# Optimization experiments

Measured on AMD Instinct MI355X. Metric: run time of the kernel, lower is better.

Reference implementation:

```python
import jax, jax.numpy as jnp
import numpy as np

QUANT_MIN = -128.0
QUANT_MAX = 127.0
EPS = 1.1920928955078125e-07  # torch.finfo(float32).eps, torchao default
STEPS = 100


def setup_inputs() -> dict:
    key = jax.random.key(0)
    x = jax.random.normal(key, (8192, 8192), dtype=jnp.float32)
    return {"x": x}


def _fake_quant_rows(x, thres):
    """Symmetric int8 fake-quant with per-row threshold.

    scale = thres / ((qmax - qmin)/2) clamped at eps, zero_point = 0.
    x: [N, K], thres: [N].
    """
    scale = jnp.maximum(thres / ((QUANT_MAX - QUANT_MIN) / 2.0), EPS)  # [N]
    s = scale[:, None]
    q = jnp.clip(jnp.round(x / s), QUANT_MIN, QUANT_MAX)
    return q * s  # dequant (zero_point == 0)


def reference(x):
    # PerAxis(axis=0): block (1, K) -> per-row stats, reduce over axis 1
    min_val = jnp.min(x, axis=1)                       # [N]
    max_val = jnp.max(x, axis=1)                       # [N]
    range_val = jnp.maximum(jnp.abs(min_val), max_val)  # [N]
    opt_loss = jnp.full_like(min_val, 1e9)

    def step(carry, i):
        min_v, max_v, opt = carry
        thres = range_val / STEPS * i                  # [N]
        xq = _fake_quant_rows(x, thres)                # [N, K]
        loss = jnp.mean(jnp.square(xq - x), axis=1)    # [N]
        better = loss < opt
        min_v = jnp.where(better, -thres, min_v)
        max_v = jnp.where(better, thres, max_v)
        opt = jnp.minimum(loss, opt)
        return (min_v, max_v, opt), None

    steps = jnp.arange(1, STEPS + 1, dtype=x.dtype)
    (min_val, max_val, _), _ = jax.lax.scan(step, (min_val, max_val, opt_loss), steps)
    return jnp.stack([min_val, max_val])  # [2, N]
```

## Files before the change

kernel.cpp:

```cpp
#include <hip/hip_runtime.h>

#define K 8192
#define NROWS 8192
#define NSTEPS 100
#define QEPS 1.1920928955078125e-07f

__global__ __launch_bounds__(256) void mse_observer_kernel(
    const float* __restrict__ x, float* __restrict__ out)
{
    const int row  = blockIdx.x;
    const int tid  = threadIdx.x;
    const int lane = tid & 63;
    const int wave = tid >> 6;

    const float4* xr = reinterpret_cast<const float4*>(x + (size_t)row * K);

    float xv[32];
    #pragma unroll
    for (int j = 0; j < 8; ++j) {
        float4 v = xr[tid + j * 256];
        xv[j * 4 + 0] = v.x;
        xv[j * 4 + 1] = v.y;
        xv[j * 4 + 2] = v.z;
        xv[j * 4 + 3] = v.w;
    }

    float vmin = xv[0], vmax = xv[0];
    #pragma unroll
    for (int e = 1; e < 32; ++e) {
        vmin = fminf(vmin, xv[e]);
        vmax = fmaxf(vmax, xv[e]);
    }
    #pragma unroll
    for (int off = 32; off >= 1; off >>= 1) {
        vmin = fminf(vmin, __shfl_xor(vmin, off));
        vmax = fmaxf(vmax, __shfl_xor(vmax, off));
    }

    __shared__ float smin[4], smax[4];
    __shared__ float partial[NSTEPS * 4];
    __shared__ float sloss[NSTEPS];

    if (lane == 0) { smin[wave] = vmin; smax[wave] = vmax; }
    __syncthreads();

    const float rmin  = fminf(fminf(smin[0], smin[1]), fminf(smin[2], smin[3]));
    const float rmax  = fmaxf(fmaxf(smax[0], smax[1]), fmaxf(smax[2], smax[3]));
    const float range = fmaxf(fabsf(rmin), rmax);
    const float rstep = range / (float)NSTEPS;

    for (int i = 1; i <= NSTEPS; ++i) {
        const float thres = rstep * (float)i;
        const float s     = fmaxf(thres / 127.5f, QEPS);
        const float inv_s = 1.0f / s;
        float acc = 0.0f;
        #pragma unroll
        for (int e = 0; e < 32; ++e) {
            float q = __builtin_amdgcn_fmed3f(
                __builtin_rintf(xv[e] * inv_s), -128.0f, 127.0f);
            float d = __builtin_fmaf(q, s, -xv[e]);
            acc = __builtin_fmaf(d, d, acc);
        }
        #pragma unroll
        for (int off = 32; off >= 1; off >>= 1) acc += __shfl_xor(acc, off);
        if (lane == 0) partial[(i - 1) * 4 + wave] = acc;
    }
    __syncthreads();

    if (tid < NSTEPS) {
        sloss[tid] = (partial[tid * 4 + 0] + partial[tid * 4 + 1]) +
                     (partial[tid * 4 + 2] + partial[tid * 4 + 3]);
    }
    __syncthreads();

    if (tid == 0) {
        float opt = 3.4e38f;
        int best = 0;
        #pragma unroll 1
        for (int i = 0; i < NSTEPS; ++i) {
            float l = sloss[i];
            if (l < opt) { opt = l; best = i; }
        }
        const float tbest = rstep * (float)(best + 1);
        out[row]         = -tbest;
        out[NROWS + row] =  tbest;
    }
}

extern "C" void kernel_launch(void* const* d_in, const int* in_sizes, int n_in,
                              void* d_out, int out_size, void* d_ws, size_t ws_size,
                              hipStream_t stream) {
    const float* x = (const float*)d_in[0];
    float* out = (float*)d_out;
    mse_observer_kernel<<<NROWS, 256, 0, stream>>>(x, out);
}
```

Baseline: 979.5 us.

## Stream row data from memory per pass over threshold chunks instead of holding it in registers

The row is no longer held in 32 registers. The 100 thresholds are split into 5 passes of 20, and each pass re-reads the row's float4 values from global memory (likely from cache) with a one-ahead prefetch. Each loaded element is reused across 20 accumulators, and the per-step scale and inverse are precomputed once into shared memory and broadcast with readfirstlane. The aim is to cut register pressure and the serialized per-step shuffle reductions, and to batch reductions so more independent work is in flight. The cost is five reloads of each row, which may add memory traffic if the cache does not hold the row.

```diff
diff --git a/kernel.cpp b/kernel.cpp
--- a/kernel.cpp
+++ b/kernel.cpp
@@ -3,7 +3,13 @@
 #define K 8192
 #define NROWS 8192
 #define NSTEPS 100
+#define CHUNK 20
+#define NPASS 5
 #define QEPS 1.1920928955078125e-07f
+
+__device__ __forceinline__ float rdfirst(float v) {
+    return __int_as_float(__builtin_amdgcn_readfirstlane(__float_as_int(v)));
+}
 
 __global__ __launch_bounds__(256) void mse_observer_kernel(
     const float* __restrict__ x, float* __restrict__ out)
@@ -13,23 +19,15 @@
     const int lane = tid & 63;
     const int wave = tid >> 6;
 
-    const float4* xr = reinterpret_cast<const float4*>(x + (size_t)row * K);
+    const float4* __restrict__ xr =
+        reinterpret_cast<const float4*>(x + (size_t)row * K);
 
-    float xv[32];
+    float vmin =  3.4e38f, vmax = -3.4e38f;
     #pragma unroll
     for (int j = 0; j < 8; ++j) {
         float4 v = xr[tid + j * 256];
-        xv[j * 4 + 0] = v.x;
-        xv[j * 4 + 1] = v.y;
-        xv[j * 4 + 2] = v.z;
-        xv[j * 4 + 3] = v.w;
-    }
-
-    float vmin = xv[0], vmax = xv[0];
-    #pragma unroll
-    for (int e = 1; e < 32; ++e) {
-        vmin = fminf(vmin, xv[e]);
-        vmax = fmaxf(vmax, xv[e]);
+        vmin = fminf(vmin, fminf(fminf(v.x, v.y), fminf(v.z, v.w)));
+        vmax = fmaxf(vmax, fmaxf(fmaxf(v.x, v.y), fmaxf(v.z, v.w)));
     }
     #pragma unroll
     for (int off = 32; off >= 1; off >>= 1) {
@@ -37,9 +35,10 @@
         vmax = fmaxf(vmax, __shfl_xor(vmax, off));
     }
 
-    __shared__ float smin[4], smax[4];
-    __shared__ float partial[NSTEPS * 4];
-    __shared__ float sloss[NSTEPS];
+    __shared__ float  smin[4], smax[4];
+    __shared__ float2 sitab[NSTEPS];
+    __shared__ float  partial[NSTEPS * 4];
+    __shared__ float  sloss[NSTEPS];
 
     if (lane == 0) { smin[wave] = vmin; smax[wave] = vmax; }
     __syncthreads();
@@ -49,21 +48,54 @@
     const float range = fmaxf(fabsf(rmin), rmax);
     const float rstep = range / (float)NSTEPS;
 
-    for (int i = 1; i <= NSTEPS; ++i) {
-        const float thres = rstep * (float)i;
+    if (tid < NSTEPS) {
+        const float thres = rstep * (float)(tid + 1);
         const float s     = fmaxf(thres / 127.5f, QEPS);
-        const float inv_s = 1.0f / s;
-        float acc = 0.0f;
+        sitab[tid] = make_float2(s, 1.0f / s);
+    }
+    __syncthreads();
+
+    #pragma unroll 1
+    for (int p = 0; p < NPASS; ++p) {
+        float ss[CHUNK], si[CHUNK];
         #pragma unroll
-        for (int e = 0; e < 32; ++e) {
-            float q = __builtin_amdgcn_fmed3f(
-                __builtin_rintf(xv[e] * inv_s), -128.0f, 127.0f);
-            float d = __builtin_fmaf(q, s, -xv[e]);
-            acc = __builtin_fmaf(d, d, acc);
+        for (int st = 0; st < CHUNK; ++st) {
+            float2 sv = sitab[p * CHUNK + st];
+            ss[st] = rdfirst(sv.x);
+            si[st] = rdfirst(sv.y);
         }
+        float acc[CHUNK];
         #pragma unroll
-        for (int off = 32; off >= 1; off >>= 1) acc += __shfl_xor(acc, off);
-        if (lane == 0) partial[(i - 1) * 4 + wave] = acc;
+        for (int st = 0; st < CHUNK; ++st) acc[st] = 0.0f;
+
+        float4 cur = xr[tid];
+        #pragma unroll 1
+        for (int j = 0; j < 8; ++j) {
+            const int jn = (j + 1) & 7;
+            float4 nxt = xr[tid + jn * 256];
+            #pragma unroll
+            for (int st = 0; st < CHUNK; ++st) {
+                const float s_ = ss[st], i_ = si[st];
+                float q, d;
+                q = __builtin_amdgcn_fmed3f(__builtin_rintf(cur.x * i_), -128.f, 127.f);
+                d = __builtin_fmaf(q, s_, -cur.x); acc[st] = __builtin_fmaf(d, d, acc[st]);
+                q = __builtin_amdgcn_fmed3f(__builtin_rintf(cur.y * i_), -128.f, 127.f);
+                d = __builtin_fmaf(q, s_, -cur.y); acc[st] = __builtin_fmaf(d, d, acc[st]);
+                q = __builtin_amdgcn_fmed3f(__builtin_rintf(cur.z * i_), -128.f, 127.f);
+                d = __builtin_fmaf(q, s_, -cur.z); acc[st] = __builtin_fmaf(d, d, acc[st]);
+                q = __builtin_amdgcn_fmed3f(__builtin_rintf(cur.w * i_), -128.f, 127.f);
+                d = __builtin_fmaf(q, s_, -cur.w); acc[st] = __builtin_fmaf(d, d, acc[st]);
+            }
+            cur = nxt;
+        }
+
+        #pragma unroll
+        for (int st = 0; st < CHUNK; ++st) {
+            float a = acc[st];
+            #pragma unroll
+            for (int off = 32; off >= 1; off >>= 1) a += __shfl_xor(a, off);
+            if (lane == 0) partial[(p * CHUNK + st) * 4 + wave] = a;
+        }
     }
     __syncthreads();
 
```

After: 1.278 ms. 30.5% more time.
